# Optimization experiments

Hardware: AMD Instinct MI355X
Metric: run time of the kernel (lower is better)

Reference implementation:

```python
import jax, jax.numpy as jnp
import numpy as np

B, C, H, W = 16, 32, 240, 240  # C=32 forced: C//2 must equal 16 pooled-query tokens
CH = C // 2


def conv1x1(x, Wt, bt):
    # 1x1 conv == per-pixel matmul over channels
    return jnp.einsum('bchw,oc->bohw', x, Wt) + bt[None, :, None, None]


def adaptive_pool6(x):
    # AdaptiveAvgPool2d((6,6)) with H,W divisible by 6 -> uniform block mean
    b, c, h, w = x.shape
    return x.reshape(b, c, 6, h // 6, 6, w // 6).mean(axis=(3, 5))


def setup_inputs() -> dict:
    key = jax.random.key(0)
    ks = jax.random.split(key, 24)
    wsc, bsc = 0.05, 0.01
    def wmat(k, o, i):
        return jax.random.normal(k, (o, i), jnp.float32) * wsc
    def bvec(k, o):
        return jax.random.normal(k, (o,), jnp.float32) * bsc
    inp = {
        'x1': jax.random.normal(ks[0], (B, C, H, W), jnp.float32),
        'x2': jax.random.normal(ks[1], (B, C, H, W), jnp.float32),
        'Wq1': wmat(ks[2], CH, C), 'bq1': bvec(ks[3], CH),
        'Wk1': wmat(ks[4], CH, C), 'bk1': bvec(ks[5], CH),
        'Wv1': wmat(ks[6], CH, C), 'bv1': bvec(ks[7], CH),
        'Wq2': wmat(ks[8], CH, C), 'bq2': bvec(ks[9], CH),
        'Wk2': wmat(ks[10], CH, C), 'bk2': bvec(ks[11], CH),
        'Wv2': wmat(ks[12], CH, C), 'bv2': bvec(ks[13], CH),
        'Wc1': wmat(ks[14], C, CH), 'bc1': bvec(ks[15], C),
        'Wc2': wmat(ks[16], C, CH), 'bc2': bvec(ks[17], C),
        # module inits gammas to 0; use small nonzero so the attention path affects output
        'gamma1': jnp.float32(0.1),
        'gamma2': jnp.float32(0.1),
    }
    return inp


def reference(x1, x2, Wq1, bq1, Wk1, bk1, Wv1, bv1, Wq2, bq2, Wk2, bk2,
              Wv2, bv2, Wc1, bc1, Wc2, bc2, gamma1, gamma2):
    b, c, h, w = x1.shape
    hw = h * w
    ch = c // 2
    # pooled queries: 6x6 adaptive pool, crop interior 4x4 -> 16 tokens
    q1 = adaptive_pool6(conv1x1(x1, Wq1, bq1))[:, :, 1:-1, 1:-1]
    q1 = q1.reshape(b, ch, 16).transpose(0, 2, 1)          # [B,16,ch]
    k1 = conv1x1(x1, Wk1, bk1).reshape(b, ch, hw)           # [B,ch,HW]
    v1 = conv1x1(x1, Wv1, bv1).reshape(b, ch, hw)
    q2 = adaptive_pool6(conv1x1(x2, Wq2, bq2))[:, :, 1:-1, 1:-1]
    q2 = q2.reshape(b, ch, 16).transpose(0, 2, 1)
    k2 = conv1x1(x2, Wk2, bk2).reshape(b, ch, hw)
    v2 = conv1x1(x2, Wv2, bv2).reshape(b, ch, hw)

    attn2 = jax.nn.softmax(jnp.einsum('bqc,bcn->bqn', q1, k2), axis=-1)  # [B,16,HW]
    out1 = (v1 * attn2).reshape(b, ch, h, w)   # elementwise (ch == 16)
    out1 = conv1x1(out1, Wc2, bc2)

    attn1 = jax.nn.softmax(jnp.einsum('bqc,bcn->bqn', q2, k1), axis=-1)
    out2 = (v2 * attn1).reshape(b, ch, h, w)
    out2 = conv1x1(out2, Wc1, bc1)

    return (x1 + gamma1 * out1, x2 + gamma2 * out2)
```

## Files before the change

### kernel.cpp

```cpp
#include <hip/hip_runtime.h>

#define HW 57600
#define BATCH 16

#define L_OFF    0
#define AT_OFF   512
#define CV_OFF   16896
#define XM_OFF   17408
#define WVT_OFF  33792

__global__ void k1a_pool(const float* __restrict__ x1, const float* __restrict__ x2,
                         float* __restrict__ ws) {
  int task = blockIdx.x * 4 + (threadIdx.x >> 6);
  int lane = threadIdx.x & 63;
  int t = task & 15, i = (task >> 4) & 31, b = (task >> 9) & 15, s = task >> 13;
  int bi = 1 + (t >> 2), bj = 1 + (t & 3);
  const float* xp = (s ? x2 : x1) + (size_t)(b * 32 + i) * HW + (40 * bi) * 240 + 40 * bj;
  float sum = 0.f;
  #pragma unroll
  for (int k = 0; k < 25; ++k) {
    int e = lane + 64 * k;
    int r = e / 40, c = e - r * 40;
    sum += xp[r * 240 + c];
  }
  #pragma unroll
  for (int off = 32; off; off >>= 1) sum += __shfl_down(sum, off);
  if (lane == 0) ws[XM_OFF + task] = sum * (1.0f / 1600.0f);
}

__global__ void k1b_fold(float* __restrict__ ws,
                         const float* __restrict__ Wq1, const float* __restrict__ bq1,
                         const float* __restrict__ Wq2, const float* __restrict__ bq2,
                         const float* __restrict__ Wk1, const float* __restrict__ bk1,
                         const float* __restrict__ Wk2, const float* __restrict__ bk2,
                         const float* __restrict__ Wv1, const float* __restrict__ Wv2) {
  int s = blockIdx.x >> 4, b = blockIdx.x & 15;
  const float* Wq = s ? Wq2 : Wq1;
  const float* bq = s ? bq2 : bq1;
  const float* Wk = s ? Wk1 : Wk2;
  const float* bk = s ? bk1 : bk2;
  __shared__ float xm[32][16];
  __shared__ float qv[16][16];
  int tid = threadIdx.x;
  for (int e = tid; e < 512; e += 256)
    xm[e >> 4][e & 15] = ws[XM_OFF + (s * 16 + b) * 512 + e];
  __syncthreads();
  {
    int t = tid >> 4, c = tid & 15;
    float acc = bq[c];
    #pragma unroll
    for (int i = 0; i < 32; ++i) acc += Wq[c * 32 + i] * xm[i][t];
    qv[t][c] = acc;
  }
  __syncthreads();
  for (int e = tid; e < 512; e += 256) {
    int i = e >> 4, t = e & 15;
    float acc = 0.f;
    #pragma unroll
    for (int c = 0; c < 16; ++c) acc += qv[t][c] * Wk[c * 32 + i];
    ws[AT_OFF + (s * 16 + b) * 512 + i * 16 + t] = acc;
  }
  if (tid < 16) {
    float acc = 0.f;
    #pragma unroll
    for (int c = 0; c < 16; ++c) acc += qv[tid][c] * bk[c];
    ws[CV_OFF + (s * 16 + b) * 16 + tid] = acc;
  }
  if (b == 0) {
    const float* Wv = s ? Wv2 : Wv1;
    for (int e = tid; e < 512; e += 256) {
      int i = e >> 4, t = e & 15;
      ws[WVT_OFF + s * 512 + i * 16 + t] = Wv[t * 32 + i];
    }
  }
}

__global__ void k2_sumexp(const float* __restrict__ x1, const float* __restrict__ x2,
                          float* __restrict__ ws) {
  int slice = blockIdx.x >> 4;
  int sub = blockIdx.x & 15;
  int s = slice >> 4, b = slice & 15;
  const float* At = ws + AT_OFF + slice * 512;
  const float* cv = ws + CV_OFF + slice * 16;
  const float* xo = (s ? x1 : x2) + (size_t)b * 32 * HW;
  float* Lp = ws + L_OFF + slice * 16;
  float La[16];
  #pragma unroll
  for (int t = 0; t < 16; ++t) La[t] = 0.f;
  for (int n = sub * 256 + (int)threadIdx.x; n < HW; n += 4096) {
    float sc[16];
    #pragma unroll
    for (int t = 0; t < 16; ++t) sc[t] = cv[t];
    #pragma unroll
    for (int i = 0; i < 32; ++i) {
      float xi = xo[(size_t)i * HW + n];
      #pragma unroll
      for (int t = 0; t < 16; ++t) sc[t] += At[i * 16 + t] * xi;
    }
    #pragma unroll
    for (int t = 0; t < 16; ++t) La[t] += __expf(sc[t]);
  }
  #pragma unroll
  for (int t = 0; t < 16; ++t) {
    float v = La[t];
    #pragma unroll
    for (int off = 32; off; off >>= 1) v += __shfl_down(v, off);
    if ((threadIdx.x & 63) == 0) atomicAdd(&Lp[t], v);
  }
}

__global__ void k2b_log(float* __restrict__ ws) {
  int e = threadIdx.x;
  float L = ws[L_OFF + e];
  ws[CV_OFF + e] -= __logf(L);
}

__global__ void k3_out(const float* __restrict__ x1, const float* __restrict__ x2,
                       const float* __restrict__ ws,
                       const float* __restrict__ Wc1, const float* __restrict__ bc1,
                       const float* __restrict__ Wc2, const float* __restrict__ bc2,
                       const float* __restrict__ bv1, const float* __restrict__ bv2,
                       const float* __restrict__ g1p, const float* __restrict__ g2p,
                       float* __restrict__ out) {
  int b = blockIdx.x / 225;
  int n = (blockIdx.x % 225) * 256 + threadIdx.x;
  const float* At1 = ws + AT_OFF + b * 512;
  const float* At2 = ws + AT_OFF + 8192 + b * 512;
  const float* cv1 = ws + CV_OFF + b * 16;
  const float* cv2 = ws + CV_OFF + 256 + b * 16;
  const float* Wv1T = ws + WVT_OFF;
  const float* Wv2T = ws + WVT_OFF + 512;
  float g1 = g1p[0], g2 = g2p[0];
  const float* x1b = x1 + (size_t)b * 32 * HW + n;
  const float* x2b = x2 + (size_t)b * 32 * HW + n;
  float xa[32], xb[32];
  #pragma unroll
  for (int i = 0; i < 32; ++i) xa[i] = x1b[(size_t)i * HW];
  #pragma unroll
  for (int i = 0; i < 32; ++i) xb[i] = x2b[(size_t)i * HW];

  float sc[16], vv[16], o16[16];
  #pragma unroll
  for (int t = 0; t < 16; ++t) { sc[t] = cv1[t]; vv[t] = bv1[t]; }
  #pragma unroll
  for (int i = 0; i < 32; ++i) {
    float a = xa[i], bx = xb[i];
    #pragma unroll
    for (int t = 0; t < 16; ++t) {
      sc[t] += At1[i * 16 + t] * bx;
      vv[t] += Wv1T[i * 16 + t] * a;
    }
  }
  #pragma unroll
  for (int t = 0; t < 16; ++t) o16[t] = vv[t] * __expf(sc[t]);
  float* out1 = out + (size_t)b * 32 * HW + n;
  #pragma unroll
  for (int o = 0; o < 32; ++o) {
    float acc = bc2[o];
    #pragma unroll
    for (int t = 0; t < 16; ++t) acc += Wc2[o * 16 + t] * o16[t];
    out1[(size_t)o * HW] = xa[o] + g1 * acc;
  }
  #pragma unroll
  for (int t = 0; t < 16; ++t) { sc[t] = cv2[t]; vv[t] = bv2[t]; }
  #pragma unroll
  for (int i = 0; i < 32; ++i) {
    float a = xa[i], bx = xb[i];
    #pragma unroll
    for (int t = 0; t < 16; ++t) {
      sc[t] += At2[i * 16 + t] * a;
      vv[t] += Wv2T[i * 16 + t] * bx;
    }
  }
  #pragma unroll
  for (int t = 0; t < 16; ++t) o16[t] = vv[t] * __expf(sc[t]);
  float* out2 = out + (size_t)(BATCH * 32) * HW + (size_t)b * 32 * HW + n;
  #pragma unroll
  for (int o = 0; o < 32; ++o) {
    float acc = bc1[o];
    #pragma unroll
    for (int t = 0; t < 16; ++t) acc += Wc1[o * 16 + t] * o16[t];
    out2[(size_t)o * HW] = xb[o] + g2 * acc;
  }
}

extern "C" void kernel_launch(void* const* d_in, const int* in_sizes, int n_in,
                              void* d_out, int out_size, void* d_ws, size_t ws_size,
                              hipStream_t stream) {
  const float* x1  = (const float*)d_in[0];
  const float* x2  = (const float*)d_in[1];
  const float* Wq1 = (const float*)d_in[2];  const float* bq1 = (const float*)d_in[3];
  const float* Wk1 = (const float*)d_in[4];  const float* bk1 = (const float*)d_in[5];
  const float* Wv1 = (const float*)d_in[6];  const float* bv1 = (const float*)d_in[7];
  const float* Wq2 = (const float*)d_in[8];  const float* bq2 = (const float*)d_in[9];
  const float* Wk2 = (const float*)d_in[10]; const float* bk2 = (const float*)d_in[11];
  const float* Wv2 = (const float*)d_in[12]; const float* bv2 = (const float*)d_in[13];
  const float* Wc1 = (const float*)d_in[14]; const float* bc1 = (const float*)d_in[15];
  const float* Wc2 = (const float*)d_in[16]; const float* bc2 = (const float*)d_in[17];
  const float* g1  = (const float*)d_in[18]; const float* g2  = (const float*)d_in[19];
  float* out = (float*)d_out;
  float* ws  = (float*)d_ws;

  hipMemsetAsync(d_ws, 0, 512 * sizeof(float), stream);
  k1a_pool<<<4096, 256, 0, stream>>>(x1, x2, ws);
  k1b_fold<<<32, 256, 0, stream>>>(ws, Wq1, bq1, Wq2, bq2, Wk1, bk1, Wk2, bk2, Wv1, Wv2);
  k2_sumexp<<<512, 256, 0, stream>>>(x1, x2, ws);
  k2b_log<<<1, 512, 0, stream>>>(ws);
  k3_out<<<3600, 256, 0, stream>>>(x1, x2, ws, Wc1, bc1, Wc2, bc2, bv1, bv2, g1, g2, out);
}
```

Measured before the change: 749.1 us.

## Vectorize loads across pool, sumexp and output kernels; stage weights in LDS

The pooling kernel now reads float4s. The sum-of-exp kernel processes four pixels per thread with float4 loads, keeps weights in shared memory, runs a block-level reduction before its atomics, and uses twice as many blocks. The output kernel processes two pixels per thread with float2 loads, stages all weights in LDS, and reloads x from global instead of holding 64 registers of inputs. The aim is wider memory transactions, fewer scalar global loads of weights, and less register pressure, at the cost of a second read of x in the output kernel and fewer threads overall.

```diff
diff --git a/kernel.cpp b/kernel.cpp
--- a/kernel.cpp
+++ b/kernel.cpp
@@ -1,6 +1,8 @@
 #include <hip/hip_runtime.h>
 
 #define HW 57600
+#define HW2 28800
+#define HW4 14400
 #define BATCH 16
 
 #define L_OFF    0
@@ -18,10 +20,13 @@
   const float* xp = (s ? x2 : x1) + (size_t)(b * 32 + i) * HW + (40 * bi) * 240 + 40 * bj;
   float sum = 0.f;
   #pragma unroll
-  for (int k = 0; k < 25; ++k) {
+  for (int k = 0; k < 7; ++k) {
     int e = lane + 64 * k;
-    int r = e / 40, c = e - r * 40;
-    sum += xp[r * 240 + c];
+    if (e < 400) {
+      int r = e / 10, c = e - r * 10;
+      float4 v = *(const float4*)(xp + r * 240 + c * 4);
+      sum += (v.x + v.y) + (v.z + v.w);
+    }
   }
   #pragma unroll
   for (int off = 32; off; off >>= 1) sum += __shfl_down(sum, off);
@@ -75,38 +80,55 @@
   }
 }
 
-__global__ void k2_sumexp(const float* __restrict__ x1, const float* __restrict__ x2,
-                          float* __restrict__ ws) {
-  int slice = blockIdx.x >> 4;
-  int sub = blockIdx.x & 15;
+__global__ __launch_bounds__(256, 4)
+void k2_sumexp(const float* __restrict__ x1, const float* __restrict__ x2,
+               float* __restrict__ ws) {
+  int slice = blockIdx.x >> 5;
+  int sub = blockIdx.x & 31;
   int s = slice >> 4, b = slice & 15;
-  const float* At = ws + AT_OFF + slice * 512;
-  const float* cv = ws + CV_OFF + slice * 16;
-  const float* xo = (s ? x1 : x2) + (size_t)b * 32 * HW;
-  float* Lp = ws + L_OFF + slice * 16;
+  __shared__ float At_s[512];
+  __shared__ float cv_s[16];
+  __shared__ float part[4][16];
+  int tid = threadIdx.x;
+  {
+    const float* At = ws + AT_OFF + slice * 512;
+    for (int e = tid; e < 512; e += 256) At_s[e] = At[e];
+    if (tid < 16) cv_s[tid] = ws[CV_OFF + slice * 16 + tid];
+  }
+  __syncthreads();
+  const float4* xo = (const float4*)((s ? x1 : x2) + (size_t)b * 32 * HW);
   float La[16];
   #pragma unroll
   for (int t = 0; t < 16; ++t) La[t] = 0.f;
-  for (int n = sub * 256 + (int)threadIdx.x; n < HW; n += 4096) {
-    float sc[16];
-    #pragma unroll
-    for (int t = 0; t < 16; ++t) sc[t] = cv[t];
+  for (int n = sub * 256 + tid; n < HW4; n += 32 * 256) {
+    float4 sc[16];
+    #pragma unroll
+    for (int t = 0; t < 16; ++t) { float c = cv_s[t]; sc[t] = make_float4(c, c, c, c); }
     #pragma unroll
     for (int i = 0; i < 32; ++i) {
-      float xi = xo[(size_t)i * HW + n];
+      float4 xi = xo[(size_t)i * HW4 + n];
       #pragma unroll
-      for (int t = 0; t < 16; ++t) sc[t] += At[i * 16 + t] * xi;
-    }
-    #pragma unroll
-    for (int t = 0; t < 16; ++t) La[t] += __expf(sc[t]);
-  }
+      for (int t = 0; t < 16; ++t) {
+        float a = At_s[i * 16 + t];
+        sc[t].x += a * xi.x; sc[t].y += a * xi.y; sc[t].z += a * xi.z; sc[t].w += a * xi.w;
+      }
+    }
+    #pragma unroll
+    for (int t = 0; t < 16; ++t)
+      La[t] += (__expf(sc[t].x) + __expf(sc[t].y)) + (__expf(sc[t].z) + __expf(sc[t].w));
+  }
+  int w = tid >> 6, lane = tid & 63;
   #pragma unroll
   for (int t = 0; t < 16; ++t) {
     float v = La[t];
     #pragma unroll
     for (int off = 32; off; off >>= 1) v += __shfl_down(v, off);
-    if ((threadIdx.x & 63) == 0) atomicAdd(&Lp[t], v);
-  }
+    if (lane == 0) part[w][t] = v;
+  }
+  __syncthreads();
+  if (tid < 16)
+    atomicAdd(ws + L_OFF + slice * 16 + tid,
+              (part[0][tid] + part[1][tid]) + (part[2][tid] + part[3][tid]));
 }
 
 __global__ void k2b_log(float* __restrict__ ws) {
@@ -115,72 +137,109 @@
   ws[CV_OFF + e] -= __logf(L);
 }
 
-__global__ void k3_out(const float* __restrict__ x1, const float* __restrict__ x2,
-                       const float* __restrict__ ws,
-                       const float* __restrict__ Wc1, const float* __restrict__ bc1,
-                       const float* __restrict__ Wc2, const float* __restrict__ bc2,
-                       const float* __restrict__ bv1, const float* __restrict__ bv2,
-                       const float* __restrict__ g1p, const float* __restrict__ g2p,
-                       float* __restrict__ out) {
-  int b = blockIdx.x / 225;
-  int n = (blockIdx.x % 225) * 256 + threadIdx.x;
-  const float* At1 = ws + AT_OFF + b * 512;
-  const float* At2 = ws + AT_OFF + 8192 + b * 512;
-  const float* cv1 = ws + CV_OFF + b * 16;
-  const float* cv2 = ws + CV_OFF + 256 + b * 16;
-  const float* Wv1T = ws + WVT_OFF;
-  const float* Wv2T = ws + WVT_OFF + 512;
-  float g1 = g1p[0], g2 = g2p[0];
-  const float* x1b = x1 + (size_t)b * 32 * HW + n;
-  const float* x2b = x2 + (size_t)b * 32 * HW + n;
-  float xa[32], xb[32];
-  #pragma unroll
-  for (int i = 0; i < 32; ++i) xa[i] = x1b[(size_t)i * HW];
-  #pragma unroll
-  for (int i = 0; i < 32; ++i) xb[i] = x2b[(size_t)i * HW];
-
-  float sc[16], vv[16], o16[16];
-  #pragma unroll
-  for (int t = 0; t < 16; ++t) { sc[t] = cv1[t]; vv[t] = bv1[t]; }
+__global__ __launch_bounds__(256, 4)
+void k3_out(const float* __restrict__ x1, const float* __restrict__ x2,
+            const float* __restrict__ ws,
+            const float* __restrict__ Wc1, const float* __restrict__ bc1,
+            const float* __restrict__ Wc2, const float* __restrict__ bc2,
+            const float* __restrict__ bv1, const float* __restrict__ bv2,
+            const float* __restrict__ g1p, const float* __restrict__ g2p,
+            float* __restrict__ out) {
+  __shared__ float At1_s[512], At2_s[512], Wv1_s[512], Wv2_s[512], Wc1_s[512], Wc2_s[512];
+  __shared__ float cv1_s[16], cv2_s[16], bv1_s[16], bv2_s[16], bc1_s[32], bc2_s[32], g_s[2];
+  int tid = threadIdx.x;
+  int b = blockIdx.y;
+  for (int e = tid; e < 512; e += 256) {
+    At1_s[e] = ws[AT_OFF + b * 512 + e];
+    At2_s[e] = ws[AT_OFF + 8192 + b * 512 + e];
+    Wv1_s[e] = ws[WVT_OFF + e];
+    Wv2_s[e] = ws[WVT_OFF + 512 + e];
+    Wc1_s[e] = Wc1[e];
+    Wc2_s[e] = Wc2[e];
+  }
+  if (tid < 16) {
+    cv1_s[tid] = ws[CV_OFF + b * 16 + tid];
+    cv2_s[tid] = ws[CV_OFF + 256 + b * 16 + tid];
+    bv1_s[tid] = bv1[tid];
+    bv2_s[tid] = bv2[tid];
+  }
+  if (tid >= 32 && tid < 64) { int o = tid - 32; bc1_s[o] = bc1[o]; bc2_s[o] = bc2[o]; }
+  if (tid == 64) { g_s[0] = g1p[0]; g_s[1] = g2p[0]; }
+  __syncthreads();
+  int n2 = blockIdx.x * 256 + tid;
+  if (n2 >= HW2) return;
+  const float2* xa = (const float2*)(x1 + (size_t)b * 32 * HW);
+  const float2* xb = (const float2*)(x2 + (size_t)b * 32 * HW);
+  float2* o1 = (float2*)(out + (size_t)b * 32 * HW);
+  float2* o2 = (float2*)(out + (size_t)(BATCH * 32) * HW + (size_t)b * 32 * HW);
+  float g1 = g_s[0], g2 = g_s[1];
+
+  float2 sc[16], vv[16];
+  #pragma unroll
+  for (int t = 0; t < 16; ++t) {
+    float c = cv1_s[t], v = bv1_s[t];
+    sc[t] = make_float2(c, c); vv[t] = make_float2(v, v);
+  }
   #pragma unroll
   for (int i = 0; i < 32; ++i) {
-    float a = xa[i], bx = xb[i];
-    #pragma unroll
-    for (int t = 0; t < 16; ++t) {
-      sc[t] += At1[i * 16 + t] * bx;
-      vv[t] += Wv1T[i * 16 + t] * a;
-    }
-  }
-  #pragma unroll
-  for (int t = 0; t < 16; ++t) o16[t] = vv[t] * __expf(sc[t]);
-  float* out1 = out + (size_t)b * 32 * HW + n;
+    float2 a  = xa[(size_t)i * HW2 + n2];
+    float2 bx = xb[(size_t)i * HW2 + n2];
+    #pragma unroll
+    for (int t = 0; t < 16; ++t) {
+      float w1 = At1_s[i * 16 + t], w2 = Wv1_s[i * 16 + t];
+      sc[t].x += w1 * bx.x; sc[t].y += w1 * bx.y;
+      vv[t].x += w2 * a.x;  vv[t].y += w2 * a.y;
+    }
+  }
+  #pragma unroll
+  for (int t = 0; t < 16; ++t) {
+    sc[t].x = vv[t].x * __expf(sc[t].x);
+    sc[t].y = vv[t].y * __expf(sc[t].y);
+  }
   #pragma unroll
   for (int o = 0; o < 32; ++o) {
-    float acc = bc2[o];
-    #pragma unroll
-    for (int t = 0; t < 16; ++t) acc += Wc2[o * 16 + t] * o16[t];
-    out1[(size_t)o * HW] = xa[o] + g1 * acc;
-  }
-  #pragma unroll
-  for (int t = 0; t < 16; ++t) { sc[t] = cv2[t]; vv[t] = bv2[t]; }
+    float bc = bc2_s[o];
+    float2 acc = make_float2(bc, bc);
+    #pragma unroll
+    for (int t = 0; t < 16; ++t) {
+      float w = Wc2_s[o * 16 + t];
+      acc.x += w * sc[t].x; acc.y += w * sc[t].y;
+    }
+    float2 xv = xa[(size_t)o * HW2 + n2];
+    o1[(size_t)o * HW2 + n2] = make_float2(xv.x + g1 * acc.x, xv.y + g1 * acc.y);
+  }
+  #pragma unroll
+  for (int t = 0; t < 16; ++t) {
+    float c = cv2_s[t], v = bv2_s[t];
+    sc[t] = make_float2(c, c); vv[t] = make_float2(v, v);
+  }
   #pragma unroll
   for (int i = 0; i < 32; ++i) {
-    float a = xa[i], bx = xb[i];
-    #pragma unroll
-    for (int t = 0; t < 16; ++t) {
-      sc[t] += At2[i * 16 + t] * a;
-      vv[t] += Wv2T[i * 16 + t] * bx;
-    }
-  }
-  #pragma unroll
-  for (int t = 0; t < 16; ++t) o16[t] = vv[t] * __expf(sc[t]);
-  float* out2 = out + (size_t)(BATCH * 32) * HW + (size_t)b * 32 * HW + n;
+    float2 a  = xa[(size_t)i * HW2 + n2];
+    float2 bx = xb[(size_t)i * HW2 + n2];
+    #pragma unroll
+    for (int t = 0; t < 16; ++t) {
+      float w1 = At2_s[i * 16 + t], w2 = Wv2_s[i * 16 + t];
+      sc[t].x += w1 * a.x;  sc[t].y += w1 * a.y;
+      vv[t].x += w2 * bx.x; vv[t].y += w2 * bx.y;
+    }
+  }
+  #pragma unroll
+  for (int t = 0; t < 16; ++t) {
+    sc[t].x = vv[t].x * __expf(sc[t].x);
+    sc[t].y = vv[t].y * __expf(sc[t].y);
+  }
   #pragma unroll
   for (int o = 0; o < 32; ++o) {
-    float acc = bc1[o];
-    #pragma unroll
-    for (int t = 0; t < 16; ++t) acc += Wc1[o * 16 + t] * o16[t];
-    out2[(size_t)o * HW] = xb[o] + g2 * acc;
+    float bc = bc1_s[o];
+    float2 acc = make_float2(bc, bc);
+    #pragma unroll
+    for (int t = 0; t < 16; ++t) {
+      float w = Wc1_s[o * 16 + t];
+      acc.x += w * sc[t].x; acc.y += w * sc[t].y;
+    }
+    float2 xv = xb[(size_t)o * HW2 + n2];
+    o2[(size_t)o * HW2 + n2] = make_float2(xv.x + g2 * acc.x, xv.y + g2 * acc.y);
   }
 }
 
@@ -204,7 +263,7 @@
   hipMemsetAsync(d_ws, 0, 512 * sizeof(float), stream);
   k1a_pool<<<4096, 256, 0, stream>>>(x1, x2, ws);
   k1b_fold<<<32, 256, 0, stream>>>(ws, Wq1, bq1, Wq2, bq2, Wk1, bk1, Wk2, bk2, Wv1, Wv2);
-  k2_sumexp<<<512, 256, 0, stream>>>(x1, x2, ws);
+  k2_sumexp<<<1024, 256, 0, stream>>>(x1, x2, ws);
   k2b_log<<<1, 512, 0, stream>>>(ws);
-  k3_out<<<3600, 256, 0, stream>>>(x1, x2, ws, Wc1, bc1, Wc2, bc2, bv1, bv2, g1, g2, out);
-}
+  k3_out<<<dim3(113, 16), 256, 0, stream>>>(x1, x2, ws, Wc1, bc1, Wc2, bc2, bv1, bv2, g1, g2, out);
+}
```

Measured after the change: 1.191 ms. 59.0% more time.
